# Kernel tuning notes

Hardware: AMD Instinct MI355X
Metric: run time of the kernel (lower is better)

Reference implementation:

```python
import jax, jax.numpy as jnp
import numpy as np
import math

N_EMBD = 1024
N_HEAD = 16
B, T = 2, 2048
MASK_VAL = -10.0  # non-standard soft mask value from original module


def setup_inputs() -> dict:
    key = jax.random.key(0)
    k1, k2, k3 = jax.random.split(key, 3)
    scale = 1.0 / math.sqrt(N_EMBD)
    x = jax.random.normal(k1, (B, T, N_EMBD), dtype=jnp.float32)
    # torch Linear weights: (out_features, in_features)
    w_attn = jax.random.normal(k2, (3 * N_EMBD, N_EMBD), dtype=jnp.float32) * scale
    w_proj = jax.random.normal(k3, (N_EMBD, N_EMBD), dtype=jnp.float32) * scale
    return {"x": x, "w_attn": w_attn, "w_proj": w_proj}


def reference(x, w_attn, w_proj):
    Bsz, Tlen, C = x.shape
    hs = C // N_HEAD
    qkv = jnp.einsum('btc,fc->btf', x, w_attn)  # [B,T,3C]
    q, k, v = jnp.split(qkv, 3, axis=-1)
    # [B,H,T,hs]
    q = q.reshape(Bsz, Tlen, N_HEAD, hs).transpose(0, 2, 1, 3)
    k = k.reshape(Bsz, Tlen, N_HEAD, hs).transpose(0, 2, 1, 3)
    v = v.reshape(Bsz, Tlen, N_HEAD, hs).transpose(0, 2, 1, 3)
    att = jnp.einsum('bhqd,bhkd->bhqk', q, k) * (1.0 / math.sqrt(hs))
    causal = jnp.tril(jnp.ones((Tlen, Tlen), dtype=bool))
    att = jnp.where(causal[None, None], att, MASK_VAL)
    att = jax.nn.softmax(att, axis=-1)
    y = jnp.einsum('bhqk,bhkd->bhqd', att, v)
    y = y.transpose(0, 2, 1, 3).reshape(Bsz, Tlen, C)
    return jnp.einsum('btc,fc->btf', y, w_proj)
```

## Files before the change

kernel.cpp:

```cpp
#include <hip/hip_runtime.h>
#include <hip/hip_bf16.h>
#include <stdint.h>

#define BSZ   2
#define TT    2048
#define NH    16
#define HS    64
#define CC    1024
#define C3    3072
#define MT    4096
#define E10   4.5399929762484854e-05f
#define SCL2  0.1803368801111204f

typedef __bf16 bf16;
typedef __bf16 bf16x8 __attribute__((ext_vector_type(8)));
typedef float  f32x4  __attribute__((ext_vector_type(4)));
typedef short  s16x4  __attribute__((ext_vector_type(4)));

#define AS1 __attribute__((address_space(1)))
#define AS3 __attribute__((address_space(3)))

__device__ __forceinline__ void glds16(const bf16* g, bf16* l) {
    __builtin_amdgcn_global_load_lds((const AS1 void*)g, (AS3 void*)l, 16, 0, 0);
}

#define NX8  (MT * CC / 8)
#define NWA8 (C3 * CC / 8)
#define NWP8 (CC * CC / 8)
__global__ __launch_bounds__(256)
void convert_all(const float* __restrict__ x, const float* __restrict__ wa,
                 const float* __restrict__ wp, bf16* __restrict__ xd,
                 bf16* __restrict__ wad, bf16* __restrict__ wpd,
                 int* __restrict__ flag) {
    __shared__ int wsum[4];
    const int tid = threadIdx.x;
    const uint16_t* x16 = (const uint16_t*)x;
    int local = 0;
    {
        uint16_t u = x16[tid];
        int e = (u >> 7) & 0xFF; local += (e >= 96 && e <= 159);
        u = x16[tid + 256];
        e = (u >> 7) & 0xFF; local += (e >= 96 && e <= 159);
    }
    local += __shfl_xor(local, 1, 64);
    local += __shfl_xor(local, 2, 64);
    local += __shfl_xor(local, 4, 64);
    local += __shfl_xor(local, 8, 64);
    local += __shfl_xor(local, 16, 64);
    local += __shfl_xor(local, 32, 64);
    if ((tid & 63) == 0) wsum[tid >> 6] = local;
    __syncthreads();
    const int cnt = wsum[0] + wsum[1] + wsum[2] + wsum[3];
    const int f = (cnt >= 461) ? 0 : 1;
    if (blockIdx.x == 0 && tid == 0) *flag = f;
    if (f == 0) return;

    long i = (long)blockIdx.x * 256 + tid;
    const float* s; bf16* d; long off;
    if (i < NX8)             { s = x;  d = xd;  off = i; }
    else if (i < NX8 + NWA8) { s = wa; d = wad; off = i - NX8; }
    else                     { s = wp; d = wpd; off = i - NX8 - NWA8; }
    const float4* sp = reinterpret_cast<const float4*>(s) + off * 2;
    float4 a = sp[0], b = sp[1];
    bf16x8 r;
    r[0] = (bf16)a.x; r[1] = (bf16)a.y; r[2] = (bf16)a.z; r[3] = (bf16)a.w;
    r[4] = (bf16)b.x; r[5] = (bf16)b.y; r[6] = (bf16)b.z; r[7] = (bf16)b.w;
    reinterpret_cast<bf16x8*>(d)[off] = r;
}

__global__ __launch_bounds__(256)
void gemm_bt(const bf16* __restrict__ A0, const bf16* __restrict__ A1,
             const bf16* __restrict__ B0, const bf16* __restrict__ B1,
             void* __restrict__ Cmain, bf16* __restrict__ Cv,
             float* __restrict__ Vtile,
             const int* __restrict__ flag,
             int M, int N, int K, int lda, int ldb, int ldc,
             int split_col, int cf32_dyn) {
    __shared__ __align__(16) char smem[33792];
    bf16* As0 = (bf16*)smem;
    bf16* Bs0 = (bf16*)(smem + 16384);

    const int f = *flag;
    const bf16* A = f ? A1 : A0;
    const bf16* B = f ? B1 : B0;
    const int cf32 = cf32_dyn & f;

    const int tid  = threadIdx.x;
    const int lane = tid & 63;
    const int wave = tid >> 6;
    const int wm   = wave >> 1;
    const int wn   = wave & 1;
    const int quad = lane >> 4;
    const int l16  = lane & 15;

    const int row0 = blockIdx.y * 128;
    const int col0 = blockIdx.x * 128;
    const bool mainblk = (split_col < 0 || col0 < split_col);

    const int srow = tid >> 2;
    const int skk  = (tid & 3) * 8;

    const bf16* Ap = A + (long)(row0 + srow) * lda + skk;
    const bf16* Bp = B + (long)(col0 + srow) * ldb + skk;

    auto stage = [&](int k0, int buf) {
        glds16(Ap + k0,                  As0 + buf * 4096 + wave * 512);
        glds16(Ap + (long)64 * lda + k0, As0 + buf * 4096 + wave * 512 + 2048);
        glds16(Bp + k0,                  Bs0 + buf * 4096 + wave * 512);
        glds16(Bp + (long)64 * ldb + k0, Bs0 + buf * 4096 + wave * 512 + 2048);
    };

    f32x4 acc[4][4] = {};
    stage(0, 0);

    for (int k0 = 0; k0 < K; k0 += 32) {
        const int buf = (k0 >> 5) & 1;
        __syncthreads();
        if (k0 + 32 < K) stage(k0 + 32, buf ^ 1);

        const bf16* Ac = As0 + buf * 4096;
        const bf16* Bc = Bs0 + buf * 4096;
        bf16x8 af[4], bfv[4];
#pragma unroll
        for (int mi = 0; mi < 4; ++mi)
            af[mi] = *reinterpret_cast<const bf16x8*>(&Ac[(wm * 64 + mi * 16 + l16) * 32 + quad * 8]);
#pragma unroll
        for (int ni = 0; ni < 4; ++ni)
            bfv[ni] = *reinterpret_cast<const bf16x8*>(&Bc[(wn * 64 + ni * 16 + l16) * 32 + quad * 8]);
#pragma unroll
        for (int mi = 0; mi < 4; ++mi)
#pragma unroll
            for (int ni = 0; ni < 4; ++ni)
                acc[mi][ni] = __builtin_amdgcn_mfma_f32_16x16x32_bf16(af[mi], bfv[ni], acc[mi][ni], 0, 0, 0);
    }

    if (mainblk) {
        if (cf32) {
#pragma unroll
            for (int mi = 0; mi < 4; ++mi)
#pragma unroll
                for (int ni = 0; ni < 4; ++ni)
#pragma unroll
                    for (int r = 0; r < 4; ++r) {
                        int row = row0 + wm * 64 + mi * 16 + quad * 4 + r;
                        int col = col0 + wn * 64 + ni * 16 + l16;
                        ((float*)Cmain)[(long)row * ldc + col] = acc[mi][ni][r];
                    }
        } else {
            __syncthreads();
            bf16* Ce = (bf16*)smem;
#pragma unroll
            for (int mi = 0; mi < 4; ++mi) {
                const int row = wm * 64 + mi * 16 + quad * 4;
#pragma unroll
                for (int ni = 0; ni < 4; ++ni) {
                    const int col = wn * 64 + ni * 16 + l16;
#pragma unroll
                    for (int r = 0; r < 4; ++r)
                        Ce[(row + r) * 132 + col] = (bf16)acc[mi][ni][r];
                }
            }
            __syncthreads();
            const int prow = tid >> 4;
            const int pc   = (tid & 15) * 8;
#pragma unroll
            for (int p = 0; p < 8; ++p) {
                const int row_l = p * 16 + prow;
                uint2 w0 = *reinterpret_cast<const uint2*>(&Ce[row_l * 132 + pc]);
                uint2 w1 = *reinterpret_cast<const uint2*>(&Ce[row_l * 132 + pc + 4]);
                uint4 w; w.x = w0.x; w.y = w0.y; w.z = w1.x; w.w = w1.y;
                *reinterpret_cast<uint4*>(
                    (bf16*)Cmain + (long)(row0 + row_l) * ldc + col0 + pc) = w;
            }
        }
    } else {
        const int h  = (col0 - split_col + wn * 64) >> 6;
        const int bq = row0 >> 11;
        const int tc = ((row0 & 2047) >> 6) + wm;
#pragma unroll
        for (int ni = 0; ni < 4; ++ni) {
            long vrow = (long)(bq * NH + h) * 64 + ni * 16 + l16;
#pragma unroll
            for (int mi = 0; mi < 4; ++mi) {
                bf16 outv[4];
#pragma unroll
                for (int r = 0; r < 4; ++r) outv[r] = (bf16)acc[mi][ni][r];
                *reinterpret_cast<uint2*>(&Cv[vrow * 2048 + tc * 64 + quad * 16 + mi * 4]) =
                    *reinterpret_cast<uint2*>(outv);
            }
        }
#pragma unroll
        for (int ni = 0; ni < 4; ++ni) {
            float s = 0.f;
#pragma unroll
            for (int mi = 0; mi < 4; ++mi)
#pragma unroll
                for (int r = 0; r < 4; ++r) s += acc[mi][ni][r];
            s += __shfl_xor(s, 16, 64);
            s += __shfl_xor(s, 32, 64);
            if (quad == 0)
                Vtile[((long)(bq * NH + h) * 32 + tc) * 64 + ni * 16 + l16] = s;
        }
    }
}

__global__ __launch_bounds__(256)
void gemm_bt64(const bf16* __restrict__ A0, const bf16* __restrict__ A1,
               const bf16* __restrict__ B0, const bf16* __restrict__ B1,
               void* __restrict__ C, const int* __restrict__ flag,
               int M, int N, int K, int lda, int ldb, int ldc, int cf32_dyn) {
    __shared__ __align__(16) char smem[34816];
    bf16* As0 = (bf16*)smem;
    bf16* Bs0 = (bf16*)(smem + 16384);

    const int f = *flag;
    const bf16* A = f ? A1 : A0;
    const bf16* B = f ? B1 : B0;
    const int cf32 = cf32_dyn & f;

    const int tid  = threadIdx.x;
    const int lane = tid & 63;
    const int wave = tid >> 6;
    const int wm   = wave >> 1;
    const int wn   = wave & 1;
    const int quad = lane >> 4;
    const int l16  = lane & 15;

    const int row0 = blockIdx.y * 128;
    const int col0 = blockIdx.x * 64;

    const int srow = tid >> 2;
    const int skk  = (tid & 3) * 8;

    const bf16* Ap = A + (long)(row0 + srow) * lda + skk;
    const bf16* Bp = B + (long)(col0 + srow) * ldb + skk;

    auto stage = [&](int k0, int buf) {
        glds16(Ap + k0,                  As0 + buf * 4096 + wave * 512);
        glds16(Ap + (long)64 * lda + k0, As0 + buf * 4096 + wave * 512 + 2048);
        glds16(Bp + k0,                  Bs0 + buf * 2048 + wave * 512);
    };

    f32x4 acc[4][2] = {};
    stage(0, 0);

    for (int k0 = 0; k0 < K; k0 += 32) {
        const int buf = (k0 >> 5) & 1;
        __syncthreads();
        if (k0 + 32 < K) stage(k0 + 32, buf ^ 1);

        const bf16* Ac = As0 + buf * 4096;
        const bf16* Bc = Bs0 + buf * 2048;
        bf16x8 af[4], bfv[2];
#pragma unroll
        for (int mi = 0; mi < 4; ++mi)
            af[mi] = *reinterpret_cast<const bf16x8*>(&Ac[(wm * 64 + mi * 16 + l16) * 32 + quad * 8]);
#pragma unroll
        for (int ni = 0; ni < 2; ++ni)
            bfv[ni] = *reinterpret_cast<const bf16x8*>(&Bc[(wn * 32 + ni * 16 + l16) * 32 + quad * 8]);
#pragma unroll
        for (int mi = 0; mi < 4; ++mi)
#pragma unroll
            for (int ni = 0; ni < 2; ++ni)
                acc[mi][ni] = __builtin_amdgcn_mfma_f32_16x16x32_bf16(af[mi], bfv[ni], acc[mi][ni], 0, 0, 0);
    }

    if (cf32) {
        __syncthreads();
        float* Ce = (float*)smem;
#pragma unroll
        for (int mi = 0; mi < 4; ++mi) {
            const int row = wm * 64 + mi * 16 + quad * 4;
#pragma unroll
            for (int ni = 0; ni < 2; ++ni) {
                const int col = wn * 32 + ni * 16 + l16;
#pragma unroll
                for (int r = 0; r < 4; ++r)
                    Ce[(row + r) * 68 + col] = acc[mi][ni][r];
            }
        }
        __syncthreads();
        const int prow = tid >> 4;
        const int pcf  = (tid & 15) * 4;
#pragma unroll
        for (int p = 0; p < 8; ++p) {
            const int row_l = p * 16 + prow;
            f32x4 w = *reinterpret_cast<const f32x4*>(&Ce[row_l * 68 + pcf]);
            *reinterpret_cast<f32x4*>(
                (float*)C + (long)(row0 + row_l) * ldc + col0 + pcf) = w;
        }
    } else {
#pragma unroll
        for (int mi = 0; mi < 4; ++mi)
#pragma unroll
            for (int ni = 0; ni < 2; ++ni)
#pragma unroll
                for (int r = 0; r < 4; ++r) {
                    int row = row0 + wm * 64 + mi * 16 + quad * 4 + r;
                    int col = col0 + wn * 32 + ni * 16 + l16;
                    ((bf16*)C)[(long)row * ldc + col] = (bf16)acc[mi][ni][r];
                }
    }
}

__global__ __launch_bounds__(256, 3)
void attn(bf16* __restrict__ qk, const bf16* __restrict__ Vt,
          const float* __restrict__ Vtile) {
    __shared__ bf16 Ks[3][64 * 64];
    __shared__ bf16 Vs[3][64 * 64];
    __shared__ float Vpart[4][64];

    const int tid  = threadIdx.x;
    const int lane = tid & 63;
    const int wave = tid >> 6;
    const int quad = lane >> 4;
    const int l16  = lane & 15;

    const int f2   = blockIdx.x;
    const int xcd  = f2 & 7;
    const int slot = f2 >> 3;
    const int u    = slot & 3;
    const int chunk = 31 - (slot >> 2);
    const int h = xcd * 2 + (u & 1);
    const int b = u >> 1;
    const int bh = b * 16 + h;
    const int q0 = chunk * 64;
    const long rbase = (long)b * TT;
    const int ktend = chunk + 1;

    const bf16* qp = qk + (rbase + q0 + wave * 16 + l16) * 2048 + h * HS;
    bf16x8 qf0 = *reinterpret_cast<const bf16x8*>(qp + quad * 8);
    bf16x8 qf1 = *reinterpret_cast<const bf16x8*>(qp + 32 + quad * 8);
#pragma unroll
    for (int j = 0; j < 8; ++j) {
        qf0[j] = (bf16)((float)qf0[j] * SCL2);
        qf1[j] = (bf16)((float)qf1[j] * SCL2);
    }

    f32x4 O[4] = {};
    f32x4 lpacc = {};
    const short one_bf16 = (short)0x3F80;
    const s16x4 ones = {one_bf16, one_bf16, one_bf16, one_bf16};
    const f32x4 FZ = {0.f, 0.f, 0.f, 0.f};

    const int rl  = lane >> 3;
    const int cs  = (lane & 7) ^ rl;
    const int row0dma = wave * 16 + rl;
    const bf16* kgb = qk + (rbase + row0dma) * 2048 + CC + h * HS + cs * 8;
    const bf16* vgb = Vt + ((long)(b * NH + h) * 64 + row0dma) * 2048 + cs * 8;
    const int sx = l16 & 7;

    auto stage = [&](int kt, int bi) {
        glds16(kgb + (long)(kt * 64) * 2048,     &Ks[bi][wave * 1024]);
        glds16(kgb + (long)(kt * 64 + 8) * 2048, &Ks[bi][wave * 1024 + 512]);
        glds16(vgb + kt * 64,                    &Vs[bi][wave * 1024]);
        glds16(vgb + 8 * 2048 + kt * 64,         &Vs[bi][wave * 1024 + 512]);
    };

    auto qkTile = [&](int bi, f32x4 (&Sn)[4]) {
        const bf16* Kc = Ks[bi];
        bf16x8 kf0[4], kf1[4];
#pragma unroll
        for (int g = 0; g < 4; ++g) {
            const int krow = g * 16 + l16;
            kf0[g] = *reinterpret_cast<const bf16x8*>(&Kc[krow * 64 + ((quad ^ sx) * 8)]);
            kf1[g] = *reinterpret_cast<const bf16x8*>(&Kc[krow * 64 + (((4 + quad) ^ sx) * 8)]);
        }
        __builtin_amdgcn_s_setprio(1);
#pragma unroll
        for (int g = 0; g < 4; ++g) {
            Sn[g] = __builtin_amdgcn_mfma_f32_16x16x32_bf16(kf0[g], qf0, FZ, 0, 0, 0);
            Sn[g] = __builtin_amdgcn_mfma_f32_16x16x32_bf16(kf1[g], qf1, Sn[g], 0, 0, 0);
        }
        __builtin_amdgcn_s_setprio(0);
    };
    auto vTile = [&](int bi, s16x4 (&vf)[4][4]) {
        const bf16* Vc = Vs[bi];
#pragma unroll
        for (int dg = 0; dg < 4; ++dg) {
            const int vrow = dg * 16 + l16;
            union { uint4 u4; s16x4 s[2]; } ua, ub;
            ua.u4 = *reinterpret_cast<const uint4*>(&Vc[vrow * 64 + (((2 * quad) ^ sx) * 8)]);
            ub.u4 = *reinterpret_cast<const uint4*>(&Vc[vrow * 64 + (((2 * quad + 1) ^ sx) * 8)]);
            vf[dg][0] = ua.s[0]; vf[dg][1] = ua.s[1];
            vf[dg][2] = ub.s[0]; vf[dg][3] = ub.s[1];
        }
    };

    f32x4 SA[4], SB[4];
    s16x4 vA[4][4], vB[4][4];

    auto body = [&](int kt, f32x4 (&Scur)[4], s16x4 (&vcur)[4][4],
                    f32x4 (&Snxt)[4], s16x4 (&vnxt)[4][4]) {
        int nkt = kt + 2; nkt = (nkt < ktend) ? nkt : (ktend - 1);
        stage(nkt, (kt + 2) % 3);
        asm volatile("s_waitcnt vmcnt(4)" ::: "memory");
        __builtin_amdgcn_s_barrier();
        __builtin_amdgcn_sched_barrier(0);

        if (kt + 1 < ktend) {
            qkTile((kt + 1) % 3, Snxt);
            vTile((kt + 1) % 3, vnxt);
        }

        const bool dtile = (kt == ktend - 1);
        const int ql = wave * 16 + l16;
        s16x4 pk[4];
#pragma unroll
        for (int g = 0; g < 4; ++g) {
#pragma unroll
            for (int r = 0; r < 4; ++r) {
                float p = __builtin_exp2f(Scur[g][r]);
                if (dtile) {
                    int kl = g * 16 + quad * 4 + r;
                    p = (kl > ql) ? E10 : p;
                }
                union { bf16 b_; short s_; } u2;
                u2.b_ = (bf16)p;
                pk[g][r] = u2.s_;
            }
        }

        __builtin_amdgcn_s_setprio(1);
#pragma unroll
        for (int dg = 0; dg < 4; ++dg) {
            O[dg] = __builtin_amdgcn_mfma_f32_16x16x16bf16_1k(vcur[dg][0], pk[0], O[dg], 0, 0, 0);
            O[dg] = __builtin_amdgcn_mfma_f32_16x16x16bf16_1k(vcur[dg][1], pk[1], O[dg], 0, 0, 0);
            O[dg] = __builtin_amdgcn_mfma_f32_16x16x16bf16_1k(vcur[dg][2], pk[2], O[dg], 0, 0, 0);
            O[dg] = __builtin_amdgcn_mfma_f32_16x16x16bf16_1k(vcur[dg][3], pk[3], O[dg], 0, 0, 0);
        }
        lpacc = __builtin_amdgcn_mfma_f32_16x16x16bf16_1k(ones, pk[0], lpacc, 0, 0, 0);
        lpacc = __builtin_amdgcn_mfma_f32_16x16x16bf16_1k(ones, pk[1], lpacc, 0, 0, 0);
        lpacc = __builtin_amdgcn_mfma_f32_16x16x16bf16_1k(ones, pk[2], lpacc, 0, 0, 0);
        lpacc = __builtin_amdgcn_mfma_f32_16x16x16bf16_1k(ones, pk[3], lpacc, 0, 0, 0);
        __builtin_amdgcn_s_setprio(0);
    };

    stage(0, 0);
    stage(ktend > 1 ? 1 : 0, 1);
    asm volatile("s_waitcnt vmcnt(4)" ::: "memory");
    __builtin_amdgcn_s_barrier();
    __builtin_amdgcn_sched_barrier(0);
    qkTile(0, SA);
    vTile(0, vA);

    int kt = 0;
    while (true) {
        body(kt, SA, vA, SB, vB);
        if (++kt >= ktend) break;
        body(kt, SB, vB, SA, vA);
        if (++kt >= ktend) break;
    }

    {
        float s = 0.f;
        for (int k2 = ktend + wave; k2 < 32; k2 += 4)
            s += Vtile[((long)bh * 32 + k2) * 64 + lane];
        Vpart[wave][lane] = s;
    }
    __syncthreads();

    const int nfut = TT - ktend * 64;
    const float l = lpacc[0] + (float)nfut * E10;
    const float invl = 1.0f / l;

    bf16* yp = qk + (rbase + q0 + wave * 16 + l16) * 2048 + h * HS;
#pragma unroll
    for (int dg = 0; dg < 4; ++dg) {
        bf16 outv[4];
#pragma unroll
        for (int r = 0; r < 4; ++r) {
            const int d = dg * 16 + quad * 4 + r;
            float vts = Vpart[0][d] + Vpart[1][d] + Vpart[2][d] + Vpart[3][d];
            float o = O[dg][r] + E10 * vts;
            outv[r] = (bf16)(o * invl);
        }
        *reinterpret_cast<uint2*>(yp + dg * 16 + quad * 4) =
            *reinterpret_cast<uint2*>(outv);
    }
}

extern "C" void kernel_launch(void* const* d_in, const int* in_sizes, int n_in,
                              void* d_out, int out_size, void* d_ws, size_t ws_size,
                              hipStream_t stream) {
    const void* x      = d_in[0];
    const void* w_attn = d_in[1];
    const void* w_proj = d_in[2];

    char* ws = (char*)d_ws;
    bf16*  qk     = (bf16*)ws;
    bf16*  Vt     = (bf16*)(ws + (size_t)MT * 2048 * 2);
    char*  p2     = ws + (size_t)MT * 2048 * 2 + (size_t)32 * 64 * 2048 * 2;
    int*   flag   = (int*)p2;
    bf16*  wp_cvt = (bf16*)(p2 + 256 + 32 * 33 * 64 * 4);
    float* Vtile  = (float*)((char*)wp_cvt + (size_t)CC * CC * 2);

    bf16* x_cvt  = (bf16*)d_out;
    bf16* wa_cvt = (bf16*)d_out + (size_t)MT * CC;

    convert_all<<<(NX8 + NWA8 + NWP8) / 256, 256, 0, stream>>>(
        (const float*)x, (const float*)w_attn, (const float*)w_proj,
        x_cvt, wa_cvt, wp_cvt, flag);

    gemm_bt<<<dim3(C3 / 128, MT / 128), 256, 0, stream>>>(
        (const bf16*)x, x_cvt, (const bf16*)w_attn, wa_cvt, qk, Vt, Vtile, flag,
        MT, C3, CC, CC, CC, 2048, 2048, 0);

    attn<<<dim3(1024), 256, 0, stream>>>(qk, Vt, Vtile);

    gemm_bt64<<<dim3(CC / 64, MT / 128), 256, 0, stream>>>(
        qk, qk, (const bf16*)w_proj, wp_cvt, d_out, flag,
        MT, CC, CC, 2048, CC, CC, 1);
}
```

Baseline: 170.8 us.

## Split QKV GEMM: new 128x256 8-wave kernel for Q/K, old kernel for V

Adds a dedicated GEMM kernel for the Q and K columns of the QKV projection. It uses 512-thread blocks with 128x256 tiles, XOR-swizzled LDS, a staged double-buffered prefetch interleaved with MFMA phases using barriers and setprio, and a grouped block ordering for L2 reuse. The original gemm_bt now runs only on the V columns through a new column offset parameter. The aim is better data reuse and overlap of memory and MFMA work for the bulk of the projection, at the cost of an extra kernel launch and larger LDS and register use.

```diff
diff --git a/kernel.cpp b/kernel.cpp
--- a/kernel.cpp
+++ b/kernel.cpp
@@ -68,6 +68,175 @@
     reinterpret_cast<bf16x8*>(d)[off] = r;
 }
 
+__global__ __launch_bounds__(512)
+void gemm8p(const bf16* __restrict__ A0, const bf16* __restrict__ A1,
+            const bf16* __restrict__ B0, const bf16* __restrict__ B1,
+            bf16* __restrict__ C, const int* __restrict__ flag) {
+    __shared__ __align__(16) bf16 smem[2 * 24576];
+
+    const int f = *flag;
+    const bf16* A = f ? A1 : A0;
+    const bf16* B = f ? B1 : B0;
+
+    const int tid  = threadIdx.x;
+    const int lane = tid & 63;
+    const int w    = tid >> 6;
+    const int wm   = w >> 2;
+    const int wn   = w & 3;
+    const int quad = lane >> 4;
+    const int l16  = lane & 15;
+    const int rl   = lane >> 3;
+    const int cs   = (lane & 7) ^ rl;
+    const int sx   = l16 & 7;
+
+    const int f2   = blockIdx.x;
+    const int wgid = (f2 & 7) * 32 + (f2 >> 3);
+    const int bx = wgid & 7, by = wgid >> 3;
+    const int row0 = by * 128, col0 = bx * 256;
+
+    const bf16* Asrc  = A + (long)(row0 + w * 16 + rl) * CC + cs * 8;
+    const bf16* Bsrc0 = B + (long)(col0 + w * 16 + rl) * CC + cs * 8;
+    const bf16* Bsrc1 = B + (long)(col0 + 128 + w * 16 + rl) * CC + cs * 8;
+
+    auto stA = [&](int t, int bi) {
+        bf16* d = smem + bi * 24576 + w * 1024;
+        glds16(Asrc + t * 64, d);
+        glds16(Asrc + (long)8 * CC + t * 64, d + 512);
+    };
+    auto stBlo = [&](int t, int bi) {
+        bf16* d = smem + bi * 24576 + 8192 + w * 1024;
+        glds16(Bsrc0 + t * 64, d);
+        glds16(Bsrc0 + (long)8 * CC + t * 64, d + 512);
+    };
+    auto stBhi = [&](int t, int bi) {
+        bf16* d = smem + bi * 24576 + 16384 + w * 1024;
+        glds16(Bsrc1 + t * 64, d);
+        glds16(Bsrc1 + (long)8 * CC + t * 64, d + 512);
+    };
+
+    auto rdA = [&](int bi, int fr, int kh) -> bf16x8 {
+        const int row = wm * 64 + fr * 16 + l16;
+        const int chk = (quad + 4 * kh) ^ sx;
+        return *reinterpret_cast<const bf16x8*>(&smem[bi * 24576 + row * 64 + chk * 8]);
+    };
+    auto rdB = [&](int bi, int cf, int kh) -> bf16x8 {
+        const int base = bi * 24576 + ((wn < 2) ? 8192 : 16384);
+        const int row = (wn & 1) * 64 + cf * 16 + l16;
+        const int chk = (quad + 4 * kh) ^ sx;
+        return *reinterpret_cast<const bf16x8*>(&smem[base + row * 64 + chk * 8]);
+    };
+
+    f32x4 acc[4][4] = {};
+    bf16x8 afA[2][2], afB[2][2], bfv[4][2];
+
+    stA(0, 0); stBlo(0, 0); stBhi(0, 0);
+
+    for (int t = 0; t < 16; ++t) {
+        const int bi = t & 1;
+        const int nx = bi ^ 1;
+        const bool pf = (t + 1 < 16);
+
+        if (pf) {
+            stA(t + 1, nx);
+            asm volatile("s_waitcnt vmcnt(2)" ::: "memory");
+        } else {
+            asm volatile("s_waitcnt vmcnt(0)" ::: "memory");
+        }
+        __builtin_amdgcn_s_barrier();
+        __builtin_amdgcn_sched_barrier(0);
+#pragma unroll
+        for (int i = 0; i < 2; ++i)
+#pragma unroll
+            for (int kh = 0; kh < 2; ++kh) {
+                afA[i][kh] = rdA(bi, i, kh);
+                bfv[i][kh] = rdB(bi, i, kh);
+            }
+        __builtin_amdgcn_s_setprio(1);
+#pragma unroll
+        for (int i = 0; i < 2; ++i)
+#pragma unroll
+            for (int j = 0; j < 2; ++j) {
+                acc[i][j] = __builtin_amdgcn_mfma_f32_16x16x32_bf16(afA[i][0], bfv[j][0], acc[i][j], 0, 0, 0);
+                acc[i][j] = __builtin_amdgcn_mfma_f32_16x16x32_bf16(afA[i][1], bfv[j][1], acc[i][j], 0, 0, 0);
+            }
+        __builtin_amdgcn_s_setprio(0);
+
+        if (pf) stBlo(t + 1, nx);
+        __builtin_amdgcn_s_barrier();
+        __builtin_amdgcn_sched_barrier(0);
+#pragma unroll
+        for (int j = 2; j < 4; ++j)
+#pragma unroll
+            for (int kh = 0; kh < 2; ++kh)
+                bfv[j][kh] = rdB(bi, j, kh);
+        __builtin_amdgcn_s_setprio(1);
+#pragma unroll
+        for (int i = 0; i < 2; ++i)
+#pragma unroll
+            for (int j = 2; j < 4; ++j) {
+                acc[i][j] = __builtin_amdgcn_mfma_f32_16x16x32_bf16(afA[i][0], bfv[j][0], acc[i][j], 0, 0, 0);
+                acc[i][j] = __builtin_amdgcn_mfma_f32_16x16x32_bf16(afA[i][1], bfv[j][1], acc[i][j], 0, 0, 0);
+            }
+        __builtin_amdgcn_s_setprio(0);
+
+        if (pf) stBhi(t + 1, nx);
+        __builtin_amdgcn_s_barrier();
+        __builtin_amdgcn_sched_barrier(0);
+#pragma unroll
+        for (int i = 0; i < 2; ++i)
+#pragma unroll
+            for (int kh = 0; kh < 2; ++kh)
+                afB[i][kh] = rdA(bi, 2 + i, kh);
+        __builtin_amdgcn_s_setprio(1);
+#pragma unroll
+        for (int i = 0; i < 2; ++i)
+#pragma unroll
+            for (int j = 2; j < 4; ++j) {
+                acc[2 + i][j] = __builtin_amdgcn_mfma_f32_16x16x32_bf16(afB[i][0], bfv[j][0], acc[2 + i][j], 0, 0, 0);
+                acc[2 + i][j] = __builtin_amdgcn_mfma_f32_16x16x32_bf16(afB[i][1], bfv[j][1], acc[2 + i][j], 0, 0, 0);
+            }
+        __builtin_amdgcn_s_setprio(0);
+
+        __builtin_amdgcn_s_barrier();
+        __builtin_amdgcn_sched_barrier(0);
+        __builtin_amdgcn_s_setprio(1);
+#pragma unroll
+        for (int i = 0; i < 2; ++i)
+#pragma unroll
+            for (int j = 0; j < 2; ++j) {
+                acc[2 + i][j] = __builtin_amdgcn_mfma_f32_16x16x32_bf16(afB[i][0], bfv[j][0], acc[2 + i][j], 0, 0, 0);
+                acc[2 + i][j] = __builtin_amdgcn_mfma_f32_16x16x32_bf16(afB[i][1], bfv[j][1], acc[2 + i][j], 0, 0, 0);
+            }
+        __builtin_amdgcn_s_setprio(0);
+    }
+
+    asm volatile("s_waitcnt vmcnt(0)" ::: "memory");
+    __builtin_amdgcn_s_barrier();
+    bf16* Ce = smem;
+#pragma unroll
+    for (int fr = 0; fr < 4; ++fr) {
+        const int row = wm * 64 + fr * 16 + quad * 4;
+#pragma unroll
+        for (int cf = 0; cf < 4; ++cf) {
+            const int col = wn * 64 + cf * 16 + l16;
+#pragma unroll
+            for (int r = 0; r < 4; ++r)
+                Ce[(row + r) * 264 + col] = (bf16)acc[fr][cf][r];
+        }
+    }
+    __builtin_amdgcn_s_barrier();
+    const int rowsel = tid >> 5;
+    const int colsel = tid & 31;
+#pragma unroll
+    for (int p = 0; p < 8; ++p) {
+        const int row_l = p * 16 + rowsel;
+        uint2 a2 = *reinterpret_cast<const uint2*>(&Ce[row_l * 264 + colsel * 8]);
+        uint2 b2 = *reinterpret_cast<const uint2*>(&Ce[row_l * 264 + colsel * 8 + 4]);
+        uint4 wv; wv.x = a2.x; wv.y = a2.y; wv.z = b2.x; wv.w = b2.y;
+        *reinterpret_cast<uint4*>(C + (long)(row0 + row_l) * 2048 + col0 + colsel * 8) = wv;
+    }
+}
+
 __global__ __launch_bounds__(256)
 void gemm_bt(const bf16* __restrict__ A0, const bf16* __restrict__ A1,
              const bf16* __restrict__ B0, const bf16* __restrict__ B1,
@@ -75,7 +244,7 @@
              float* __restrict__ Vtile,
              const int* __restrict__ flag,
              int M, int N, int K, int lda, int ldb, int ldc,
-             int split_col, int cf32_dyn) {
+             int split_col, int cf32_dyn, int col_base) {
     __shared__ __align__(16) char smem[33792];
     bf16* As0 = (bf16*)smem;
     bf16* Bs0 = (bf16*)(smem + 16384);
@@ -94,7 +263,7 @@
     const int l16  = lane & 15;
 
     const int row0 = blockIdx.y * 128;
-    const int col0 = blockIdx.x * 128;
+    const int col0 = blockIdx.x * 128 + col_base;
     const bool mainblk = (split_col < 0 || col0 < split_col);
 
     const int srow = tid >> 2;
@@ -168,9 +337,9 @@
                 const int row_l = p * 16 + prow;
                 uint2 w0 = *reinterpret_cast<const uint2*>(&Ce[row_l * 132 + pc]);
                 uint2 w1 = *reinterpret_cast<const uint2*>(&Ce[row_l * 132 + pc + 4]);
-                uint4 w; w.x = w0.x; w.y = w0.y; w.z = w1.x; w.w = w1.y;
+                uint4 wv; wv.x = w0.x; wv.y = w0.y; wv.z = w1.x; wv.w = w1.y;
                 *reinterpret_cast<uint4*>(
-                    (bf16*)Cmain + (long)(row0 + row_l) * ldc + col0 + pc) = w;
+                    (bf16*)Cmain + (long)(row0 + row_l) * ldc + col0 + pc) = wv;
             }
         }
     } else {
@@ -285,9 +454,9 @@
 #pragma unroll
         for (int p = 0; p < 8; ++p) {
             const int row_l = p * 16 + prow;
-            f32x4 w = *reinterpret_cast<const f32x4*>(&Ce[row_l * 68 + pcf]);
+            f32x4 wv = *reinterpret_cast<const f32x4*>(&Ce[row_l * 68 + pcf]);
             *reinterpret_cast<f32x4*>(
-                (float*)C + (long)(row0 + row_l) * ldc + col0 + pcf) = w;
+                (float*)C + (long)(row0 + row_l) * ldc + col0 + pcf) = wv;
         }
     } else {
 #pragma unroll
@@ -502,9 +671,12 @@
         (const float*)x, (const float*)w_attn, (const float*)w_proj,
         x_cvt, wa_cvt, wp_cvt, flag);
 
-    gemm_bt<<<dim3(C3 / 128, MT / 128), 256, 0, stream>>>(
+    gemm8p<<<dim3(256), 512, 0, stream>>>(
+        (const bf16*)x, x_cvt, (const bf16*)w_attn, wa_cvt, qk, flag);
+
+    gemm_bt<<<dim3(8, MT / 128), 256, 0, stream>>>(
         (const bf16*)x, x_cvt, (const bf16*)w_attn, wa_cvt, qk, Vt, Vtile, flag,
-        MT, C3, CC, CC, CC, 2048, 2048, 0);
+        MT, C3, CC, CC, CC, 2048, 2048, 0, 2048);
 
     attn<<<dim3(1024), 256, 0, stream>>>(qk, Vt, Vtile);
 
```

Measured after the change: 179.1 us. 1.05x slower.
